# Kernel optimization log

Measured on AMD Instinct MI355X. Metric: run time of the kernel, lower is better.

The kernel has to match this reference:

```python
import jax, jax.numpy as jnp
import numpy as np

B, S, R, Z, NLHS = 1024, 277, 76, 56, 24  # batch, seq_len, n_rules, z_size, n_lhs_symbols


def setup_inputs() -> dict:
    key = jax.random.key(0)
    k1, k2, k3, k4, k5, k6 = jax.random.split(key, 6)
    model_out_x = jax.random.normal(k1, (B, S, R), jnp.float32)
    mu = jax.random.normal(k2, (B, Z), jnp.float32)
    log_var = 0.1 * jax.random.normal(k3, (B, Z), jnp.float32)
    # one-hot targets over rules
    tgt_idx = jax.random.randint(k4, (B, S), 0, R)
    target_x = jax.nn.one_hot(tgt_idx, R, dtype=jnp.float32)
    # binary allowed-transition masks per LHS symbol
    masks = (jax.random.uniform(k5, (NLHS, R)) < 0.3).astype(jnp.float32)
    masks = masks.at[:, 0].set(1.0)  # ensure no all-zero mask row
    ind_to_lhs_ind = jax.random.randint(k6, (R,), 0, NLHS)
    return dict(model_out_x=model_out_x, mu=mu, log_var=log_var,
                target_x=target_x, masks=masks, ind_to_lhs_ind=ind_to_lhs_ind)


def reference(model_out_x, mu, log_var, target_x, masks, ind_to_lhs_ind):
    b = model_out_x.shape[0]
    seq_len = model_out_x.shape[1]
    z_size = mu.shape[1]

    # --- apply_masks: vectorized gather replacing the nested python loops ---
    true_rule = jnp.argmax(target_x, axis=-1)          # [B,S]
    lhs = ind_to_lhs_ind[true_rule]                    # [B,S]
    mask = masks[lhs]                                  # [B,S,R]
    shift_to_tiny = -100.0 + (model_out_x.min() - model_out_x.max())
    x = model_out_x + (1.0 - mask) * shift_to_tiny

    # --- softmax + BCE (torch BCELoss clamps log terms at -100) ---
    p = jax.nn.softmax(x, axis=-1)
    log_p = jnp.maximum(jnp.log(p), -100.0)
    log_1mp = jnp.maximum(jnp.log1p(-p), -100.0)
    bce = -jnp.mean(target_x * log_p + (1.0 - target_x) * log_1mp)
    BCE = seq_len * bce

    # --- moment-matching error on mu ---
    avg_mu = jnp.sum(mu, axis=0) / b                   # [Z]
    var = (mu.T @ mu) / b                              # [Z,Z]
    var_err = var - jnp.eye(z_size, dtype=mu.dtype)
    var_err = jnp.tanh(var_err) * var_err
    mom_err = jnp.sum(avg_mu * avg_mu) / z_size + jnp.sum(var_err) / (z_size * z_size)

    # sample_z=False, module in training mode -> loss = BCE + mom_err
    return BCE + mom_err
```

## Files before the change

kernel.cpp:

```cpp
#include <hip/hip_runtime.h>
#include <math.h>

#define BB    1024
#define SS    277
#define RR    76
#define ZZ    56
#define NLHS  24
#define NROWS (BB*SS)
#define ROWS_PER_BLOCK 256
#define NBCE (NROWS/ROWS_PER_BLOCK)
#define NMOM ZZ
#define NBLK (NBCE + NMOM)
#define V4_PER_BLOCK (ROWS_PER_BLOCK*RR/4)
#define BLK_ELEMS (ROWS_PER_BLOCK*RR)
#define TOTAL_ELEMS 21558272.0

static_assert(NROWS % ROWS_PER_BLOCK == 0, "rows divide blocks");

#define LN2F  0.69314718056f
#define NLN2F (-144.26950409f)

__device__ __forceinline__ float keep(float v) {
    asm volatile("" : "+v"(v));
    return v;
}

__global__ __launch_bounds__(256, 4) void fused_kernel(
    const float* __restrict__ model,
    const float* __restrict__ target,
    const float* __restrict__ masks,
    const int*   __restrict__ ind_to_lhs,
    const float* __restrict__ mu,
    double* __restrict__ partials)
{
    __shared__ unsigned int  smb[NLHS*4];
    __shared__ int           sm_lhs[RR];
    __shared__ unsigned char sm_idx[ROWS_PER_BLOCK];
    __shared__ float         sm_red[4];
    __shared__ float         sdot[4][64];
    __shared__ float         ssum[4];

    const int tid = threadIdx.x;

    if (blockIdx.x < NMOM) {
        const int j    = blockIdx.x;
        const int w    = tid >> 6;
        const int lane = tid & 63;
        const int i    = (lane < ZZ) ? lane : 0;
        float dot = 0.f, s1 = 0.f;
        const int b0 = 256*w;
        #pragma unroll 4
        for (int b = b0; b < b0 + 256; ++b) {
            const float c = mu[b*ZZ + j];
            const float a = mu[b*ZZ + i];
            dot = fmaf(a, c, dot);
            s1 += c;
        }
        sdot[w][lane] = dot;
        if (lane == 0) ssum[w] = s1;
        __syncthreads();
        if (w == 0) {
            float term = 0.f;
            if (lane < ZZ) {
                const float var = (sdot[0][lane]+sdot[1][lane]+sdot[2][lane]+sdot[3][lane]) * (1.f/BB);
                const float ve  = var - ((lane == j) ? 1.f : 0.f);
                term = tanhf(ve) * ve * (1.f/(ZZ*ZZ));
                if (lane == j) {
                    const float am = (ssum[0]+ssum[1]+ssum[2]+ssum[3]) * (1.f/BB);
                    term = fmaf(am*am, 1.f/ZZ, term);
                }
            }
            #pragma unroll
            for (int off = 32; off; off >>= 1) term += __shfl_xor(term, off, 64);
            if (lane == 0) partials[blockIdx.x] = (double)term;
        }
        return;
    }

    const int bce_blk = blockIdx.x - NMOM;

    if (tid < NLHS*4) smb[tid] = 0u;
    sm_idx[tid] = 0;
    __syncthreads();

    for (int e = tid; e < NLHS*RR; e += 256) {
        const int lhs = e / RR;
        const int r   = e - lhs*RR;
        if (masks[e] > 0.5f)
            atomicOr(&smb[lhs*4 + (r >> 5)], 1u << (r & 31));
    }
    if (tid < RR) sm_lhs[tid] = ind_to_lhs[tid];

    const size_t blk_base = (size_t)bce_blk * BLK_ELEMS;

    const float4* m4 = (const float4*)(model + blk_base + (size_t)tid * RR);
    float4 x[19];
    #pragma unroll
    for (int k = 0; k < 19; ++k) x[k] = m4[k];

    {
        const float4* t4 = (const float4*)(target + blk_base);
        #pragma unroll
        for (int k = 0; k < 19; ++k) {
            const int v4 = tid + 256*k;
            const float4 t = t4[v4];
            int he = -1;
            const int e = v4*4;
            if (t.x > 0.5f) he = e;
            if (t.y > 0.5f) he = e+1;
            if (t.z > 0.5f) he = e+2;
            if (t.w > 0.5f) he = e+3;
            if (he >= 0) {
                const int row = he / RR;
                sm_idx[row] = (unsigned char)(he - row*RR);
            }
        }
    }
    __syncthreads();

    #pragma unroll
    for (int k = 0; k < 19; ++k) {
        x[k].x = keep(x[k].x); x[k].y = keep(x[k].y);
        x[k].z = keep(x[k].z); x[k].w = keep(x[k].w);
    }

    const int true_r = (int)sm_idx[tid];
    const int lhs    = sm_lhs[true_r];
    const unsigned int mw0 = smb[lhs*4 + 0];
    const unsigned int mw1 = smb[lhs*4 + 1];
    const unsigned int mw2 = smb[lhs*4 + 2];

    float mx = -1e30f;
    #pragma unroll
    for (int k = 0; k < 19; ++k) {
        #pragma unroll
        for (int c = 0; c < 4; ++c) {
            const int r = k*4 + c;
            const unsigned int mw = (r < 32) ? mw0 : ((r < 64) ? mw1 : mw2);
            float* xp = (&x[k].x) + c;
            const bool un = (mw >> (r & 31)) & 1u;
            const float xm = un ? *xp : -1e30f;
            *xp = xm;
            mx = fmaxf(mx, xm);
        }
    }

    float s = 0.f;
    #pragma unroll
    for (int k = 0; k < 19; ++k) {
        #pragma unroll
        for (int c = 0; c < 4; ++c) {
            float* xp = (&x[k].x) + c;
            const float e = __expf(*xp - mx);
            *xp = e;
            s += e;
        }
    }

    const float inv = 1.f / s;
    float sum_l2 = 0.f;
    float p_true = 0.f;
    #pragma unroll
    for (int k = 0; k < 19; ++k) {
        #pragma unroll
        for (int c = 0; c < 4; ++c) {
            const int r = k*4 + c;
            const float p  = (&x[k].x)[c] * inv;
            const float l2 = __log2f(1.f - p);
            sum_l2 += fmaxf(l2, NLN2F);
            if (r == true_r) p_true = p;
        }
    }
    float row_sum = LN2F * sum_l2;
    const float l1c_t = fmaxf(LN2F * __log2f(1.f - p_true), -100.f);
    const float lp_t  = fmaxf(__logf(p_true), -100.f);
    row_sum += lp_t - l1c_t;

    #pragma unroll
    for (int off = 32; off; off >>= 1) row_sum += __shfl_xor(row_sum, off, 64);
    if ((tid & 63) == 0) sm_red[tid >> 6] = row_sum;
    __syncthreads();
    if (tid == 0)
        partials[blockIdx.x] = (double)((sm_red[0] + sm_red[1]) + (sm_red[2] + sm_red[3]));
}

__global__ __launch_bounds__(256) void final_kernel(
    const double* __restrict__ partials, float* __restrict__ out)
{
    __shared__ double sred[4];
    const int tid = threadIdx.x;
    double s = 0.0;
    for (int k = NMOM + tid; k < NBLK; k += 256) s += partials[k];
    double m = (tid < NMOM) ? partials[tid] : 0.0;
    double val = s * (-(double)SS / TOTAL_ELEMS) + m;
    #pragma unroll
    for (int off = 32; off; off >>= 1) val += __shfl_xor(val, off, 64);
    if ((tid & 63) == 0) sred[tid >> 6] = val;
    __syncthreads();
    if (tid == 0) out[0] = (float)((sred[0] + sred[1]) + (sred[2] + sred[3]));
}

extern "C" void kernel_launch(void* const* d_in, const int* in_sizes, int n_in,
                              void* d_out, int out_size, void* d_ws, size_t ws_size,
                              hipStream_t stream) {
    const float* model  = (const float*)d_in[0];
    const float* mu     = (const float*)d_in[1];
    const float* target = (const float*)d_in[3];
    const float* masks  = (const float*)d_in[4];
    const int*   ind    = (const int*)  d_in[5];
    float* out  = (float*)d_out;
    double* acc = (double*)d_ws;

    fused_kernel<<<NBLK, ROWS_PER_BLOCK, 0, stream>>>(model, target, masks, ind, mu, acc);
    final_kernel<<<1, 256, 0, stream>>>(acc, out);
}
```

Measured before the change: 214.1 us.

## Stage model rows through LDS via async global_load_lds and recompute exp

Model logits are now copied into a 77KB shared-memory tile with coalesced global_load_lds instructions instead of each thread loading its own strided 304-byte row into registers. Each row is then read back from LDS in three passes, and exp is recomputed in the final pass rather than kept in registers. This aims to improve global coalescing and overlap the loads with the mask and target setup. The cost is lower occupancy (launch bounds drop to 2, LDS-limited), extra LDS traffic with strided row access that may cause bank conflicts, and recomputed exponentials.

```diff
diff --git a/kernel.cpp b/kernel.cpp
--- a/kernel.cpp
+++ b/kernel.cpp
@@ -11,7 +11,8 @@
 #define NBCE (NROWS/ROWS_PER_BLOCK)
 #define NMOM ZZ
 #define NBLK (NBCE + NMOM)
-#define V4_PER_BLOCK (ROWS_PER_BLOCK*RR/4)
+#define F4ROW 19
+#define F4BLK (ROWS_PER_BLOCK*F4ROW)
 #define BLK_ELEMS (ROWS_PER_BLOCK*RR)
 #define TOTAL_ELEMS 21558272.0
 
@@ -20,12 +21,15 @@
 #define LN2F  0.69314718056f
 #define NLN2F (-144.26950409f)
 
-__device__ __forceinline__ float keep(float v) {
-    asm volatile("" : "+v"(v));
-    return v;
-}
-
-__global__ __launch_bounds__(256, 4) void fused_kernel(
+__device__ __forceinline__ void gload_lds16(const float4* g, float4* l) {
+    auto gp = reinterpret_cast<const __attribute__((address_space(1))) unsigned int*>(
+        reinterpret_cast<uintptr_t>(g));
+    auto lp = reinterpret_cast<__attribute__((address_space(3))) unsigned int*>(
+        reinterpret_cast<uintptr_t>(l));
+    __builtin_amdgcn_global_load_lds(gp, lp, 16, 0, 0);
+}
+
+__global__ __launch_bounds__(256, 2) void fused_kernel(
     const float* __restrict__ model,
     const float* __restrict__ target,
     const float* __restrict__ masks,
@@ -33,6 +37,7 @@
     const float* __restrict__ mu,
     double* __restrict__ partials)
 {
+    __shared__ float4        sx[F4BLK];
     __shared__ unsigned int  smb[NLHS*4];
     __shared__ int           sm_lhs[RR];
     __shared__ unsigned char sm_idx[ROWS_PER_BLOCK];
@@ -78,10 +83,24 @@
     }
 
     const int bce_blk = blockIdx.x - NMOM;
+    const size_t blk_base = (size_t)bce_blk * BLK_ELEMS;
 
     if (tid < NLHS*4) smb[tid] = 0u;
     sm_idx[tid] = 0;
     __syncthreads();
+
+    float4 t[F4ROW];
+    {
+        const float4* t4 = (const float4*)(target + blk_base);
+        #pragma unroll
+        for (int k = 0; k < F4ROW; ++k) t[k] = t4[tid + 256*k];
+    }
+    {
+        const float4* g4 = (const float4*)(model + blk_base);
+        #pragma unroll
+        for (int k = 0; k < F4ROW; ++k)
+            gload_lds16(g4 + tid + 256*k, &sx[tid + 256*k]);
+    }
 
     for (int e = tid; e < NLHS*RR; e += 256) {
         const int lhs = e / RR;
@@ -91,38 +110,22 @@
     }
     if (tid < RR) sm_lhs[tid] = ind_to_lhs[tid];
 
-    const size_t blk_base = (size_t)bce_blk * BLK_ELEMS;
-
-    const float4* m4 = (const float4*)(model + blk_base + (size_t)tid * RR);
-    float4 x[19];
-    #pragma unroll
-    for (int k = 0; k < 19; ++k) x[k] = m4[k];
-
-    {
-        const float4* t4 = (const float4*)(target + blk_base);
-        #pragma unroll
-        for (int k = 0; k < 19; ++k) {
-            const int v4 = tid + 256*k;
-            const float4 t = t4[v4];
-            int he = -1;
-            const int e = v4*4;
-            if (t.x > 0.5f) he = e;
-            if (t.y > 0.5f) he = e+1;
-            if (t.z > 0.5f) he = e+2;
-            if (t.w > 0.5f) he = e+3;
-            if (he >= 0) {
-                const int row = he / RR;
-                sm_idx[row] = (unsigned char)(he - row*RR);
-            }
-        }
-    }
-    __syncthreads();
-
-    #pragma unroll
-    for (int k = 0; k < 19; ++k) {
-        x[k].x = keep(x[k].x); x[k].y = keep(x[k].y);
-        x[k].z = keep(x[k].z); x[k].w = keep(x[k].w);
-    }
+    #pragma unroll
+    for (int k = 0; k < F4ROW; ++k) {
+        const int v4 = tid + 256*k;
+        const float4 tv = t[k];
+        int he = -1;
+        const int e = v4*4;
+        if (tv.x > 0.5f) he = e;
+        if (tv.y > 0.5f) he = e+1;
+        if (tv.z > 0.5f) he = e+2;
+        if (tv.w > 0.5f) he = e+3;
+        if (he >= 0) {
+            const int row = he / RR;
+            sm_idx[row] = (unsigned char)(he - row*RR);
+        }
+    }
+    __syncthreads();
 
     const int true_r = (int)sm_idx[tid];
     const int lhs    = sm_lhs[true_r];
@@ -130,30 +133,33 @@
     const unsigned int mw1 = smb[lhs*4 + 1];
     const unsigned int mw2 = smb[lhs*4 + 2];
 
+    const float4* xr = &sx[tid*F4ROW];
+
     float mx = -1e30f;
     #pragma unroll
-    for (int k = 0; k < 19; ++k) {
+    for (int k = 0; k < F4ROW; ++k) {
+        const float4 v = xr[k];
         #pragma unroll
         for (int c = 0; c < 4; ++c) {
             const int r = k*4 + c;
             const unsigned int mw = (r < 32) ? mw0 : ((r < 64) ? mw1 : mw2);
-            float* xp = (&x[k].x) + c;
             const bool un = (mw >> (r & 31)) & 1u;
-            const float xm = un ? *xp : -1e30f;
-            *xp = xm;
+            const float xm = un ? (&v.x)[c] : -1e30f;
             mx = fmaxf(mx, xm);
         }
     }
 
     float s = 0.f;
     #pragma unroll
-    for (int k = 0; k < 19; ++k) {
+    for (int k = 0; k < F4ROW; ++k) {
+        const float4 v = xr[k];
         #pragma unroll
         for (int c = 0; c < 4; ++c) {
-            float* xp = (&x[k].x) + c;
-            const float e = __expf(*xp - mx);
-            *xp = e;
-            s += e;
+            const int r = k*4 + c;
+            const unsigned int mw = (r < 32) ? mw0 : ((r < 64) ? mw1 : mw2);
+            const bool un = (mw >> (r & 31)) & 1u;
+            const float xm = un ? (&v.x)[c] : -1e30f;
+            s += __expf(xm - mx);
         }
     }
 
@@ -161,11 +167,16 @@
     float sum_l2 = 0.f;
     float p_true = 0.f;
     #pragma unroll
-    for (int k = 0; k < 19; ++k) {
+    for (int k = 0; k < F4ROW; ++k) {
+        const float4 v = xr[k];
         #pragma unroll
         for (int c = 0; c < 4; ++c) {
             const int r = k*4 + c;
-            const float p  = (&x[k].x)[c] * inv;
+            const unsigned int mw = (r < 32) ? mw0 : ((r < 64) ? mw1 : mw2);
+            const bool un = (mw >> (r & 31)) & 1u;
+            const float xm = un ? (&v.x)[c] : -1e30f;
+            const float ev = __expf(xm - mx);
+            const float p  = ev * inv;
             const float l2 = __log2f(1.f - p);
             sum_l2 += fmaxf(l2, NLN2F);
             if (r == true_r) p_true = p;
```

Result: no change. 215.4 us (+0.6%).
